# Performance work log

Hardware: AMD Instinct MI355X
Metric: run time of the kernel (lower is better)

## Reference

```python
import jax, jax.numpy as jnp
import numpy as np
import math

B, S, HID = 2, 2048, 2048
H, HK, D = 16, 4, 128          # query heads, kv heads, head_dim
R = 64                         # rope_dim = head_dim * partial_rotary_factor
EPS = 1e-6
THETA = 10000.0


def _rope_tables():
    inv_freq = 1.0 / (THETA ** (np.arange(0, R, 2, dtype=np.float32) / R))
    t = np.arange(S, dtype=np.float32)
    freqs = np.outer(t, inv_freq)                      # [S, R/2]
    emb = np.concatenate([freqs, freqs], axis=-1)      # [S, R]
    cos = np.broadcast_to(np.cos(emb)[None], (B, S, R)).copy()
    sin = np.broadcast_to(np.sin(emb)[None], (B, S, R)).copy()
    return jnp.asarray(cos), jnp.asarray(sin)


def setup_inputs() -> dict:
    key = jax.random.key(0)
    ks = jax.random.split(key, 3)
    cos, sin = _rope_tables()
    return {
        "hidden_states": jax.random.normal(ks[0], (B, S, HID), dtype=jnp.float32),
        "cos": cos,
        "sin": sin,
        "w_qkv": jax.random.normal(ks[1], ((H + 2 * HK) * D, HID), dtype=jnp.float32) * (HID ** -0.5),
        "q_ln_w": jnp.ones((D,), dtype=jnp.float32),
        "k_ln_w": jnp.ones((D,), dtype=jnp.float32),
        "w_dense": jax.random.normal(ks[2], (HID, H * D), dtype=jnp.float32) * ((H * D) ** -0.5),
    }


def _rms_norm(x, w):
    xf = x.astype(jnp.float32)
    var = jnp.mean(xf * xf, axis=-1, keepdims=True)
    return w * (xf * jax.lax.rsqrt(var + EPS)).astype(x.dtype)


def _rotate_half(x):
    x1, x2 = x[..., : x.shape[-1] // 2], x[..., x.shape[-1] // 2 :]
    return jnp.concatenate([-x2, x1], axis=-1)


def _apply_rope(q, k, cos, sin):
    # cos/sin: [B, S, R] -> [B, 1, S, R]; partial rotary on first R dims
    cos = cos[:, None, :, :]
    sin = sin[:, None, :, :]
    q_rot, q_pass = q[..., :R], q[..., R:]
    k_rot, k_pass = k[..., :R], k[..., R:]
    q_emb = q_rot * cos + _rotate_half(q_rot) * sin
    k_emb = k_rot * cos + _rotate_half(k_rot) * sin
    return (jnp.concatenate([q_emb, q_pass], axis=-1),
            jnp.concatenate([k_emb, k_pass], axis=-1))


def reference(hidden_states, cos, sin, w_qkv, q_ln_w, k_ln_w, w_dense):
    bsz, q_len, _ = hidden_states.shape
    qkv = jnp.einsum('bsh,oh->bso', hidden_states, w_qkv)            # [B,S,(H+2HK)*D]
    qkv = qkv.reshape(bsz, q_len, H + 2 * HK, D)
    q, k, v = jnp.split(qkv, [H, H + HK], axis=2)
    q = jnp.transpose(q, (0, 2, 1, 3))                               # [B,H,S,D]
    k = jnp.transpose(k, (0, 2, 1, 3))                               # [B,HK,S,D]
    v = jnp.transpose(v, (0, 2, 1, 3))

    q = _rms_norm(q, q_ln_w)
    k = _rms_norm(k, k_ln_w)
    q, k = _apply_rope(q, k, cos, sin)

    n_rep = H // HK
    k = jnp.repeat(k, n_rep, axis=1)                                 # [B,H,S,D]
    v = jnp.repeat(v, n_rep, axis=1)

    scores = jnp.einsum('bhqd,bhkd->bhqk', q, k) / math.sqrt(D)
    probs = jax.nn.softmax(scores.astype(jnp.float32), axis=-1).astype(q.dtype)
    attn = jnp.einsum('bhqk,bhkd->bhqd', probs, v)                   # [B,H,S,D]
    attn = jnp.transpose(attn, (0, 2, 1, 3)).reshape(bsz, q_len, H * D)
    return jnp.einsum('bsd,od->bso', attn, w_dense)                  # [B,S,HID]
```

## Files before the change

kernel.cpp:

```cpp
#include <hip/hip_runtime.h>
#include <hip/hip_bf16.h>
#include <math.h>

#define B_   2
#define S_   2048
#define HID_ 2048
#define H_   16
#define HK_  4
#define D_   128
#define NH_  24
#define QKVN 3072
#define R_   64

typedef __attribute__((ext_vector_type(8))) _Float16 h8;
typedef __attribute__((ext_vector_type(4))) _Float16 h4;
typedef __attribute__((ext_vector_type(2))) _Float16 h2;
typedef __attribute__((ext_vector_type(4))) float f4;

#define GLOAD16(gp, lp) __builtin_amdgcn_global_load_lds(                      \
    (const __attribute__((address_space(1))) void*)(gp),                       \
    (__attribute__((address_space(3))) void*)(lp), 16, 0, 0)

__global__ __launch_bounds__(256) void cvt3(
    const float* __restrict__ s0, _Float16* __restrict__ d0, int n0,
    const float* __restrict__ s1, _Float16* __restrict__ d1, int n1,
    const float* __restrict__ s2, _Float16* __restrict__ d2, int n2)
{
    int j = blockIdx.x * 256 + threadIdx.x;
    const float* s; _Float16* d;
    if (j < n0) { s = s0; d = d0; }
    else {
        j -= n0;
        if (j < n1) { s = s1; d = d1; }
        else { j -= n1; if (j >= n2) return; s = s2; d = d2; }
    }
    float4 a = ((const float4*)s)[j * 2];
    float4 b = ((const float4*)s)[j * 2 + 1];
    h8 h;
    h[0] = (_Float16)a.x; h[1] = (_Float16)a.y;
    h[2] = (_Float16)a.z; h[3] = (_Float16)a.w;
    h[4] = (_Float16)b.x; h[5] = (_Float16)b.y;
    h[6] = (_Float16)b.z; h[7] = (_Float16)b.w;
    ((h8*)d)[j] = h;
}

template<bool F16OUT>
__global__ __launch_bounds__(256) void gemm_f16(
    const _Float16* __restrict__ A, const _Float16* __restrict__ Bm,
    void* __restrict__ Cv, int M, int N, int K)
{
    __shared__ _Float16 Ast[128][64];
    __shared__ _Float16 Bst[128][64];

    const int tid = threadIdx.x;
    const int wave = tid >> 6, lane = tid & 63;
    const int l15 = lane & 15, l4 = lane >> 4;
    const int m0 = blockIdx.y * 128, n0 = blockIdx.x * 128;
    const int wm = (wave >> 1) * 64, wn = (wave & 1) * 64;

    f4 acc[16];
#pragma unroll
    for (int t = 0; t < 16; ++t) acc[t] = (f4){0.f, 0.f, 0.f, 0.f};

    const int srow = lane >> 3;
    const int scol = ((lane & 7) ^ srow) * 8;
    const int sw   = l15 & 7;

    for (int k0 = 0; k0 < K; k0 += 64) {
        __syncthreads();
#pragma unroll
        for (int t = 0; t < 4; ++t) {
            const int chunk = wave * 4 + t;
            const int grow  = chunk * 8 + srow;
            GLOAD16(A  + (size_t)(m0 + grow) * K + k0 + scol, &Ast[chunk * 8][0]);
            GLOAD16(Bm + (size_t)(n0 + grow) * K + k0 + scol, &Bst[chunk * 8][0]);
        }
        __syncthreads();

#pragma unroll
        for (int j = 0; j < 2; ++j) {
            h8 ahf[4], bhf[4];
#pragma unroll
            for (int i = 0; i < 4; ++i) {
                ahf[i] = *(const h8*)&Ast[wm + i * 16 + l15][((j * 4 + l4) ^ sw) * 8];
                bhf[i] = *(const h8*)&Bst[wn + i * 16 + l15][((j * 4 + l4) ^ sw) * 8];
            }
#pragma unroll
            for (int i = 0; i < 4; ++i)
#pragma unroll
                for (int jj = 0; jj < 4; ++jj)
                    acc[i * 4 + jj] = __builtin_amdgcn_mfma_f32_16x16x32_f16(
                        ahf[i], bhf[jj], acc[i * 4 + jj], 0, 0, 0);
        }
    }

#pragma unroll
    for (int i = 0; i < 4; ++i)
#pragma unroll
        for (int jj = 0; jj < 4; ++jj)
#pragma unroll
            for (int r = 0; r < 4; ++r) {
                int row = m0 + wm + i * 16 + l4 * 4 + r;
                int col = n0 + wn + jj * 16 + l15;
                if (F16OUT)
                    ((_Float16*)Cv)[(size_t)row * N + col] = (_Float16)acc[i * 4 + jj][r];
                else
                    ((float*)Cv)[(size_t)row * N + col] = acc[i * 4 + jj][r];
            }
}

__global__ __launch_bounds__(256) void norm_rope(
    const _Float16* __restrict__ qkv,
    const float* __restrict__ cosT, const float* __restrict__ sinT,
    const float* __restrict__ qw, const float* __restrict__ kw,
    _Float16* __restrict__ Qh_g, _Float16* __restrict__ Kh_g)
{
    const int tid = threadIdx.x;
    const int wave = tid >> 6, lane = tid & 63;
    const int h = blockIdx.x * 4 + wave;
    const int s = blockIdx.y, b = blockIdx.z;
    const size_t tok = (size_t)b * S_ + s;

    h2 xv = *(const h2*)(qkv + (tok * NH_ + h) * D_ + 2 * lane);
    float x0 = (float)xv[0], x1 = (float)xv[1];
    float ss = x0 * x0 + x1 * x1;
    ss += __shfl_xor(ss, 1);  ss += __shfl_xor(ss, 2);  ss += __shfl_xor(ss, 4);
    ss += __shfl_xor(ss, 8);  ss += __shfl_xor(ss, 16); ss += __shfl_xor(ss, 32);
    float scale = rsqrtf(ss * (1.f / 128.f) + 1e-6f);

    const float* wp = (h < 16) ? qw : kw;
    float2 wv = ((const float2*)wp)[lane];
    float y0 = x0 * scale * wv.x;
    float y1 = x1 * scale * wv.y;

    float p0 = __shfl_xor(y0, 16), p1 = __shfl_xor(y1, 16);
    if (lane < 32) {
        float2 cv = ((const float2*)(cosT + tok * R_))[lane];
        float2 sv = ((const float2*)(sinT + tok * R_))[lane];
        float sgn = (lane < 16) ? -1.f : 1.f;
        y0 = y0 * cv.x + sgn * p0 * sv.x;
        y1 = y1 * cv.y + sgn * p1 * sv.y;
    }

    if (h < 16) {
        const float QS = 0.08838834764831845f * 1.4426950408889634f;
        h2 o; o[0] = (_Float16)(y0 * QS); o[1] = (_Float16)(y1 * QS);
        *(h2*)(Qh_g + (((size_t)b * H_ + h) * S_ + s) * D_ + 2 * lane) = o;
    } else {
        h2 o; o[0] = (_Float16)y0; o[1] = (_Float16)y1;
        *(h2*)(Kh_g + (((size_t)b * HK_ + (h - 16)) * S_ + s) * D_ + 2 * lane) = o;
    }
}

__global__ __launch_bounds__(256) void vtrans(
    const _Float16* __restrict__ qkv, _Float16* __restrict__ Vt_g)
{
    __shared__ float Ts[64][132];
    const int tid = threadIdx.x;
    const int sb = blockIdx.x;
    const int bh = blockIdx.y;
    const int b = bh >> 2, kh = bh & 3;

#pragma unroll
    for (int t = 0; t < 4; ++t) {
        int e = (tid + 256 * t) * 8;
        int s = e >> 7, d = e & 127;
        const _Float16* p = qkv + (((size_t)(b * S_ + sb * 64 + s)) * NH_ + 20 + kh) * D_ + d;
        h8 v = *(const h8*)p;
#pragma unroll
        for (int u = 0; u < 8; ++u) Ts[s][d + u] = (float)v[u];
    }
    __syncthreads();

#pragma unroll
    for (int tt = 0; tt < 2; ++tt) {
        int dr = (tid >> 2) + 64 * tt;
        int sc = (tid & 3) * 16;
        _Float16 tmp[16];
#pragma unroll
        for (int i = 0; i < 16; ++i) tmp[i] = (_Float16)Ts[sc + i][dr];
        _Float16* outp = Vt_g + ((size_t)bh * D_ + dr) * S_ + sb * 64 + sc;
        *(h8*)outp       = *(h8*)&tmp[0];
        *(h8*)(outp + 8) = *(h8*)&tmp[8];
    }
}

__global__ __launch_bounds__(256, 2) void flash_mfma(
    const _Float16* __restrict__ Qh_g, const _Float16* __restrict__ Kh_g,
    const _Float16* __restrict__ Vt_g, _Float16* __restrict__ Ao)
{
    __shared__ _Float16 Ksh[2][64][128];
    __shared__ _Float16 Vsh[2][128][64];
    __shared__ _Float16 Ps [128][64];

    const int tid = threadIdx.x;
    const int wave = tid >> 6, lane = tid & 63;
    const int l15 = lane & 15, l4 = lane >> 4;
    const int qb = blockIdx.x, h = blockIdx.y, b = blockIdx.z;
    const int kh = h >> 2;
    const int key = l15 & 7;

    h8 qf[2][4];
#pragma unroll
    for (int i = 0; i < 2; ++i) {
        const _Float16* qrow = Qh_g +
            (((size_t)b * H_ + h) * S_ + qb * 128 + wave * 32 + i * 16 + l15) * D_;
#pragma unroll
        for (int j = 0; j < 4; ++j)
            qf[i][j] = *(const h8*)(qrow + j * 32 + l4 * 8);
    }

    f4 o[2][8];
#pragma unroll
    for (int i = 0; i < 2; ++i)
#pragma unroll
        for (int t = 0; t < 8; ++t) o[i][t] = (f4){0.f, 0.f, 0.f, 0.f};
    float l_part[2] = {0.f, 0.f};

    const size_t kvoff = ((size_t)b * HK_ + kh) * S_ * D_;
    const _Float16* kg = Kh_g + kvoff;
    const _Float16* vg = Vt_g + kvoff;

    int krow[4], ksrc[4], vrow[4], vsrc[4];
#pragma unroll
    for (int t = 0; t < 4; ++t) {
        krow[t] = wave * 16 + t * 4 + (lane >> 4);
        ksrc[t] = ((lane & 15) ^ (krow[t] & 7)) * 8;
        vrow[t] = wave * 32 + t * 8 + (lane >> 3);
        vsrc[t] = ((lane & 7) ^ (vrow[t] & 7)) * 8;
    }

    auto STAGE = [&](int bf, int kb) {
#pragma unroll
        for (int t = 0; t < 4; ++t)
            GLOAD16(kg + (size_t)(kb * 64 + krow[t]) * D_ + ksrc[t],
                    &Ksh[bf][wave * 16 + t * 4][0]);
#pragma unroll
        for (int t = 0; t < 4; ++t)
            GLOAD16(vg + (size_t)vrow[t] * S_ + kb * 64 + vsrc[t],
                    &Vsh[bf][wave * 32 + t * 8][0]);
    };

    STAGE(0, 0);
    int cur = 0;

    for (int kb = 0; kb < S_ / 64; ++kb) {
        __syncthreads();
        if (kb + 1 < S_ / 64) STAGE(cur ^ 1, kb + 1);

        f4 acc[4][2];
#pragma unroll
        for (int c = 0; c < 4; ++c)
#pragma unroll
            for (int i = 0; i < 2; ++i)
                acc[c][i] = (f4){-8.f, -8.f, -8.f, -8.f};
#pragma unroll
        for (int j = 0; j < 4; ++j) {
#pragma unroll
            for (int c = 0; c < 4; ++c) {
                h8 kf = *(const h8*)&Ksh[cur][c * 16 + l15][((j * 4 + l4) ^ key) * 8];
#pragma unroll
                for (int i = 0; i < 2; ++i)
                    acc[c][i] = __builtin_amdgcn_mfma_f32_16x16x32_f16(
                        kf, qf[i][j], acc[c][i], 0, 0, 0);
            }
        }

#pragma unroll
        for (int c = 0; c < 4; ++c) {
#pragma unroll
            for (int i = 0; i < 2; ++i) {
                h4 pk;
#pragma unroll
                for (int r = 0; r < 4; ++r) {
                    float e_ = exp2f(acc[c][i][r]);
                    l_part[i] += e_;
                    pk[r] = (_Float16)e_;
                }
                int g = 2 * c + (l4 >> 1);
                *(h4*)&Ps[wave * 32 + i * 16 + l15][(g ^ key) * 8 + (l4 & 1) * 4] = pk;
            }
        }

#pragma unroll
        for (int s2 = 0; s2 < 2; ++s2) {
            int gc = ((s2 * 4 + l4) ^ key) * 8;
            h8 pf0 = *(const h8*)&Ps[wave * 32 + l15][gc];
            h8 pf1 = *(const h8*)&Ps[wave * 32 + 16 + l15][gc];
#pragma unroll
            for (int t = 0; t < 8; ++t) {
                h8 vf = *(const h8*)&Vsh[cur][t * 16 + l15][gc];
                o[0][t] = __builtin_amdgcn_mfma_f32_16x16x32_f16(pf0, vf, o[0][t], 0, 0, 0);
                o[1][t] = __builtin_amdgcn_mfma_f32_16x16x32_f16(pf1, vf, o[1][t], 0, 0, 0);
            }
        }
        cur ^= 1;
    }

    float Linv[2];
#pragma unroll
    for (int i = 0; i < 2; ++i) {
        float l = l_part[i];
        l += __shfl_xor(l, 16);
        l += __shfl_xor(l, 32);
        Linv[i] = 1.f / l;
    }
#pragma unroll
    for (int i = 0; i < 2; ++i) {
        float inv[4];
#pragma unroll
        for (int r = 0; r < 4; ++r) inv[r] = __shfl(Linv[i], l4 * 4 + r);
#pragma unroll
        for (int t = 0; t < 8; ++t) {
#pragma unroll
            for (int r = 0; r < 4; ++r) {
                int row = qb * 128 + wave * 32 + i * 16 + l4 * 4 + r;
                Ao[((size_t)b * S_ + row) * (H_ * D_) + h * D_ + t * 16 + l15] =
                    (_Float16)(o[i][t][r] * inv[r]);
            }
        }
    }
}

extern "C" void kernel_launch(void* const* d_in, const int* in_sizes, int n_in,
                              void* d_out, int out_size, void* d_ws, size_t ws_size,
                              hipStream_t stream)
{
    const float* hidden  = (const float*)d_in[0];
    const float* cosT    = (const float*)d_in[1];
    const float* sinT    = (const float*)d_in[2];
    const float* w_qkv   = (const float*)d_in[3];
    const float* q_ln    = (const float*)d_in[4];
    const float* k_ln    = (const float*)d_in[5];
    const float* w_dense = (const float*)d_in[6];
    float* out = (float*)d_out;

    char* w = (char*)d_ws;
    _Float16* qkv16 = (_Float16*)w;
    _Float16* Qh    = (_Float16*)(w + 25165824);
    _Float16* Kh    = (_Float16*)(w + 41943040);
    _Float16* Vt    = (_Float16*)(w + 46137344);
    _Float16* wdense16 = (_Float16*)(w + 54525952);
    _Float16* hidden16 = Qh;
    _Float16* wqkv16   = Kh;
    _Float16* attn16   = qkv16;

    cvt3<<<9216, 256, 0, stream>>>(hidden,  hidden16, 1048576,
                                   w_qkv,   wqkv16,   786432,
                                   w_dense, wdense16, 524288);

    gemm_f16<true><<<dim3(QKVN / 128, (B_ * S_) / 128), 256, 0, stream>>>(
        hidden16, wqkv16, qkv16, B_ * S_, QKVN, HID_);

    norm_rope<<<dim3(5, S_, B_), 256, 0, stream>>>(
        qkv16, cosT, sinT, q_ln, k_ln, Qh, Kh);

    vtrans<<<dim3(S_ / 64, B_ * HK_), 256, 0, stream>>>(qkv16, Vt);

    flash_mfma<<<dim3(S_ / 128, H_, B_), 256, 0, stream>>>(Qh, Kh, Vt, attn16);

    gemm_f16<false><<<dim3(HID_ / 128, (B_ * S_) / 128), 256, 0, stream>>>(
        attn16, wdense16, out, B_ * S_, HID_, H_ * D_);
}
```

Measured before the change: 354.5 us.

## Split flash attention waves across query and key halves with LDS reduction

The flash kernel now splits its four waves as 2 query groups x 2 key groups. Each wave covers 64 query rows and 32 of the 64 keys per block, so each Q fragment is reused against more K/V loads, and the two key-half partial outputs and row sums are combined through shared memory at the end. The GEMM inner loop also raises wave priority around the MFMA burst. The trade-off is more live accumulator registers per wave (o grows from 16 to 32 f4), which may lower occupancy or cause spills, plus an extra LDS reduction and barrier in the epilogue.

After: 375.0 us. 1.06x slower.

```diff
diff --git a/kernel.cpp b/kernel.cpp
--- a/kernel.cpp
+++ b/kernel.cpp
@@ -85,12 +85,14 @@
                 ahf[i] = *(const h8*)&Ast[wm + i * 16 + l15][((j * 4 + l4) ^ sw) * 8];
                 bhf[i] = *(const h8*)&Bst[wn + i * 16 + l15][((j * 4 + l4) ^ sw) * 8];
             }
+            __builtin_amdgcn_s_setprio(1);
 #pragma unroll
             for (int i = 0; i < 4; ++i)
 #pragma unroll
                 for (int jj = 0; jj < 4; ++jj)
                     acc[i * 4 + jj] = __builtin_amdgcn_mfma_f32_16x16x32_f16(
                         ahf[i], bhf[jj], acc[i * 4 + jj], 0, 0, 0);
+            __builtin_amdgcn_s_setprio(0);
         }
     }
 
@@ -189,33 +191,35 @@
     const _Float16* __restrict__ Qh_g, const _Float16* __restrict__ Kh_g,
     const _Float16* __restrict__ Vt_g, _Float16* __restrict__ Ao)
 {
-    __shared__ _Float16 Ksh[2][64][128];
-    __shared__ _Float16 Vsh[2][128][64];
-    __shared__ _Float16 Ps [128][64];
+    __shared__ char smem[81920];
+    auto Ksh = (_Float16 (*)[64][128])smem;
+    auto Vsh = (_Float16 (*)[128][64])(smem + 32768);
+    auto Ps  = (_Float16 (*)[64])(smem + 65536);
 
     const int tid = threadIdx.x;
     const int wave = tid >> 6, lane = tid & 63;
     const int l15 = lane & 15, l4 = lane >> 4;
+    const int wq = wave >> 1, wk = wave & 1;
     const int qb = blockIdx.x, h = blockIdx.y, b = blockIdx.z;
     const int kh = h >> 2;
     const int key = l15 & 7;
 
-    h8 qf[2][4];
-#pragma unroll
-    for (int i = 0; i < 2; ++i) {
+    h8 qf[4][4];
+#pragma unroll
+    for (int i = 0; i < 4; ++i) {
         const _Float16* qrow = Qh_g +
-            (((size_t)b * H_ + h) * S_ + qb * 128 + wave * 32 + i * 16 + l15) * D_;
+            (((size_t)b * H_ + h) * S_ + qb * 128 + wq * 64 + i * 16 + l15) * D_;
 #pragma unroll
         for (int j = 0; j < 4; ++j)
             qf[i][j] = *(const h8*)(qrow + j * 32 + l4 * 8);
     }
 
-    f4 o[2][8];
-#pragma unroll
-    for (int i = 0; i < 2; ++i)
+    f4 o[4][8];
+#pragma unroll
+    for (int i = 0; i < 4; ++i)
 #pragma unroll
         for (int t = 0; t < 8; ++t) o[i][t] = (f4){0.f, 0.f, 0.f, 0.f};
-    float l_part[2] = {0.f, 0.f};
+    float l_part[4] = {0.f, 0.f, 0.f, 0.f};
 
     const size_t kvoff = ((size_t)b * HK_ + kh) * S_ * D_;
     const _Float16* kg = Kh_g + kvoff;
@@ -248,28 +252,29 @@
         __syncthreads();
         if (kb + 1 < S_ / 64) STAGE(cur ^ 1, kb + 1);
 
-        f4 acc[4][2];
-#pragma unroll
-        for (int c = 0; c < 4; ++c)
-#pragma unroll
-            for (int i = 0; i < 2; ++i)
+        f4 acc[2][4];
+#pragma unroll
+        for (int c = 0; c < 2; ++c)
+#pragma unroll
+            for (int i = 0; i < 4; ++i)
                 acc[c][i] = (f4){-8.f, -8.f, -8.f, -8.f};
 #pragma unroll
         for (int j = 0; j < 4; ++j) {
 #pragma unroll
-            for (int c = 0; c < 4; ++c) {
-                h8 kf = *(const h8*)&Ksh[cur][c * 16 + l15][((j * 4 + l4) ^ key) * 8];
-#pragma unroll
-                for (int i = 0; i < 2; ++i)
+            for (int c = 0; c < 2; ++c) {
+                h8 kf = *(const h8*)&Ksh[cur][wk * 32 + c * 16 + l15]
+                                          [((j * 4 + l4) ^ key) * 8];
+#pragma unroll
+                for (int i = 0; i < 4; ++i)
                     acc[c][i] = __builtin_amdgcn_mfma_f32_16x16x32_f16(
                         kf, qf[i][j], acc[c][i], 0, 0, 0);
             }
         }
 
 #pragma unroll
-        for (int c = 0; c < 4; ++c) {
-#pragma unroll
-            for (int i = 0; i < 2; ++i) {
+        for (int c = 0; c < 2; ++c) {
+#pragma unroll
+            for (int i = 0; i < 4; ++i) {
                 h4 pk;
 #pragma unroll
                 for (int r = 0; r < 4; ++r) {
@@ -277,47 +282,71 @@
                     l_part[i] += e_;
                     pk[r] = (_Float16)e_;
                 }
-                int g = 2 * c + (l4 >> 1);
-                *(h4*)&Ps[wave * 32 + i * 16 + l15][(g ^ key) * 8 + (l4 & 1) * 4] = pk;
-            }
-        }
-
-#pragma unroll
-        for (int s2 = 0; s2 < 2; ++s2) {
-            int gc = ((s2 * 4 + l4) ^ key) * 8;
-            h8 pf0 = *(const h8*)&Ps[wave * 32 + l15][gc];
-            h8 pf1 = *(const h8*)&Ps[wave * 32 + 16 + l15][gc];
+                int g = wk * 4 + c * 2 + (l4 >> 1);
+                *(h4*)&Ps[wq * 64 + i * 16 + l15][(g ^ key) * 8 + (l4 & 1) * 4] = pk;
+            }
+        }
+
+        {
+            const int gc = ((wk * 4 + l4) ^ key) * 8;
+            h8 pf[4];
+#pragma unroll
+            for (int i = 0; i < 4; ++i)
+                pf[i] = *(const h8*)&Ps[wq * 64 + i * 16 + l15][gc];
 #pragma unroll
             for (int t = 0; t < 8; ++t) {
                 h8 vf = *(const h8*)&Vsh[cur][t * 16 + l15][gc];
-                o[0][t] = __builtin_amdgcn_mfma_f32_16x16x32_f16(pf0, vf, o[0][t], 0, 0, 0);
-                o[1][t] = __builtin_amdgcn_mfma_f32_16x16x32_f16(pf1, vf, o[1][t], 0, 0, 0);
+#pragma unroll
+                for (int i = 0; i < 4; ++i)
+                    o[i][t] = __builtin_amdgcn_mfma_f32_16x16x32_f16(
+                        pf[i], vf, o[i][t], 0, 0, 0);
             }
         }
         cur ^= 1;
     }
 
-    float Linv[2];
-#pragma unroll
-    for (int i = 0; i < 2; ++i) {
+    float lp[4];
+#pragma unroll
+    for (int i = 0; i < 4; ++i) {
         float l = l_part[i];
         l += __shfl_xor(l, 16);
         l += __shfl_xor(l, 32);
-        Linv[i] = 1.f / l;
-    }
-#pragma unroll
-    for (int i = 0; i < 2; ++i) {
-        float inv[4];
-#pragma unroll
-        for (int r = 0; r < 4; ++r) inv[r] = __shfl(Linv[i], l4 * 4 + r);
-#pragma unroll
-        for (int t = 0; t < 8; ++t) {
-#pragma unroll
-            for (int r = 0; r < 4; ++r) {
-                int row = qb * 128 + wave * 32 + i * 16 + l4 * 4 + r;
-                Ao[((size_t)b * S_ + row) * (H_ * D_) + h * D_ + t * 16 + l15] =
-                    (_Float16)(o[i][t][r] * inv[r]);
-            }
+        lp[i] = l;
+    }
+
+    __syncthreads();
+    float (*ex)[128] = (float (*)[128])smem;
+    float* Ls = (float*)(smem + 65536);
+
+    if (wk == 1) {
+#pragma unroll
+        for (int i = 0; i < 4; ++i) {
+#pragma unroll
+            for (int t = 0; t < 8; ++t)
+#pragma unroll
+                for (int r = 0; r < 4; ++r)
+                    ex[wq * 64 + i * 16 + l4 * 4 + r][t * 16 + l15] = o[i][t][r];
+            if (l4 == 0) Ls[wq * 64 + i * 16 + l15] = lp[i];
+        }
+    }
+    __syncthreads();
+    if (wk == 0) {
+#pragma unroll
+        for (int i = 0; i < 4; ++i) {
+            float Linv = 1.f / (lp[i] + Ls[wq * 64 + i * 16 + l15]);
+            float inv[4];
+#pragma unroll
+            for (int r = 0; r < 4; ++r) inv[r] = __shfl(Linv, l4 * 4 + r);
+#pragma unroll
+            for (int t = 0; t < 8; ++t)
+#pragma unroll
+                for (int r = 0; r < 4; ++r) {
+                    int qrow = wq * 64 + i * 16 + l4 * 4 + r;
+                    int row = qb * 128 + qrow;
+                    float v = o[i][t][r] + ex[qrow][t * 16 + l15];
+                    Ao[((size_t)b * S_ + row) * (H_ * D_) + h * D_ + t * 16 + l15] =
+                        (_Float16)(v * inv[r]);
+                }
         }
     }
 }
```

## Fuse RMSNorm, RoPE and V transpose into QKV GEMM epilogue

Applied to the files above, without the earlier changes.

The QKV projection GEMM now normalizes each head tile in its epilogue. It reduces the squared sums across the two N-half waves through shared memory, then applies RoPE and the query scale before writing Q/K in head-major layout. It also writes V directly transposed. This drops the separate norm_rope and vtrans kernels and the fp16 qkv intermediate round-trip. The change also adds s_setprio around the MFMA blocks in both GEMMs, and the epilogue writes Q/K with scattered 2-byte stores, which may be less coalesced than before.

New measurement: 335.7 us. -5.3%, faster.

```diff
diff --git a/kernel.cpp b/kernel.cpp
--- a/kernel.cpp
+++ b/kernel.cpp
@@ -44,10 +44,166 @@
     ((h8*)d)[j] = h;
 }
 
-template<bool F16OUT>
-__global__ __launch_bounds__(256) void gemm_f16(
+__global__ __launch_bounds__(256) void gemm_qkv(
     const _Float16* __restrict__ A, const _Float16* __restrict__ Bm,
-    void* __restrict__ Cv, int M, int N, int K)
+    const float* __restrict__ cosT, const float* __restrict__ sinT,
+    const float* __restrict__ qw, const float* __restrict__ kw,
+    _Float16* __restrict__ Qh_g, _Float16* __restrict__ Kh_g,
+    _Float16* __restrict__ Vt_g)
+{
+    __shared__ _Float16 Ast[128][64];
+    __shared__ _Float16 Bst[128][64];
+    __shared__ float exch[2][128];
+
+    const int tid = threadIdx.x;
+    const int wave = tid >> 6, lane = tid & 63;
+    const int l15 = lane & 15, l4 = lane >> 4;
+    const int h  = blockIdx.x;
+    const int m0 = blockIdx.y * 128;
+    const int n0 = h * 128;
+    const int wm = (wave >> 1) * 64, wn = (wave & 1) * 64;
+    const int K = HID_;
+
+    f4 acc[16];
+#pragma unroll
+    for (int t = 0; t < 16; ++t) acc[t] = (f4){0.f, 0.f, 0.f, 0.f};
+
+    const int srow = lane >> 3;
+    const int scol = ((lane & 7) ^ srow) * 8;
+    const int sw   = l15 & 7;
+
+    for (int k0 = 0; k0 < K; k0 += 64) {
+        __syncthreads();
+#pragma unroll
+        for (int t = 0; t < 4; ++t) {
+            const int chunk = wave * 4 + t;
+            const int grow  = chunk * 8 + srow;
+            GLOAD16(A  + (size_t)(m0 + grow) * K + k0 + scol, &Ast[chunk * 8][0]);
+            GLOAD16(Bm + (size_t)(n0 + grow) * K + k0 + scol, &Bst[chunk * 8][0]);
+        }
+        __syncthreads();
+
+#pragma unroll
+        for (int j = 0; j < 2; ++j) {
+            h8 ahf[4], bhf[4];
+#pragma unroll
+            for (int i = 0; i < 4; ++i) {
+                ahf[i] = *(const h8*)&Ast[wm + i * 16 + l15][((j * 4 + l4) ^ sw) * 8];
+                bhf[i] = *(const h8*)&Bst[wn + i * 16 + l15][((j * 4 + l4) ^ sw) * 8];
+            }
+            __builtin_amdgcn_s_setprio(1);
+#pragma unroll
+            for (int i = 0; i < 4; ++i)
+#pragma unroll
+                for (int jj = 0; jj < 4; ++jj)
+                    acc[i * 4 + jj] = __builtin_amdgcn_mfma_f32_16x16x32_f16(
+                        ahf[i], bhf[jj], acc[i * 4 + jj], 0, 0, 0);
+            __builtin_amdgcn_s_setprio(0);
+        }
+    }
+
+    const int bb = m0 >> 11;
+    const int s0 = m0 & 2047;
+
+    if (h < 20) {
+        float sq[4][4];
+#pragma unroll
+        for (int i = 0; i < 4; ++i)
+#pragma unroll
+            for (int r = 0; r < 4; ++r) {
+                float s = 0.f;
+#pragma unroll
+                for (int jj = 0; jj < 4; ++jj) {
+                    float v = acc[i * 4 + jj][r];
+                    s += v * v;
+                }
+                s += __shfl_xor(s, 1);
+                s += __shfl_xor(s, 2);
+                s += __shfl_xor(s, 4);
+                s += __shfl_xor(s, 8);
+                sq[i][r] = s;
+            }
+        const int half = wn >> 6;
+        if (l15 == 0) {
+#pragma unroll
+            for (int i = 0; i < 4; ++i)
+#pragma unroll
+                for (int r = 0; r < 4; ++r)
+                    exch[half][wm + i * 16 + l4 * 4 + r] = sq[i][r];
+        }
+        __syncthreads();
+
+        const float* wln = (h < 16) ? qw : kw;
+        float wv[4];
+#pragma unroll
+        for (int jj = 0; jj < 4; ++jj) wv[jj] = wln[wn + jj * 16 + l15];
+
+        const float QS = 0.08838834764831845f * 1.4426950408889634f;
+
+#pragma unroll
+        for (int i = 0; i < 4; ++i) {
+#pragma unroll
+            for (int r = 0; r < 4; ++r) {
+                const int row = wm + i * 16 + l4 * 4 + r;
+                const int s  = s0 + row;
+                float tot = sq[i][r] + exch[half ^ 1][row];
+                float scale = rsqrtf(tot * (1.f / 128.f) + 1e-6f);
+                float y[4];
+#pragma unroll
+                for (int jj = 0; jj < 4; ++jj)
+                    y[jj] = acc[i * 4 + jj][r] * scale * wv[jj];
+
+                float yr[4];
+                if (wn == 0) {
+                    const float* cp = cosT + ((size_t)bb * S_ + s) * R_;
+                    const float* sp = sinT + ((size_t)bb * S_ + s) * R_;
+                    float cs[4], sn[4];
+#pragma unroll
+                    for (int jj = 0; jj < 4; ++jj) {
+                        cs[jj] = cp[jj * 16 + l15];
+                        sn[jj] = sp[jj * 16 + l15];
+                    }
+                    yr[0] = y[0] * cs[0] - y[2] * sn[0];
+                    yr[1] = y[1] * cs[1] - y[3] * sn[1];
+                    yr[2] = y[2] * cs[2] + y[0] * sn[2];
+                    yr[3] = y[3] * cs[3] + y[1] * sn[3];
+                } else {
+#pragma unroll
+                    for (int jj = 0; jj < 4; ++jj) yr[jj] = y[jj];
+                }
+
+                if (h < 16) {
+                    _Float16* qp = Qh_g + (((size_t)bb * H_ + h) * S_ + s) * D_;
+#pragma unroll
+                    for (int jj = 0; jj < 4; ++jj)
+                        qp[wn + jj * 16 + l15] = (_Float16)(yr[jj] * QS);
+                } else {
+                    _Float16* kp = Kh_g + (((size_t)bb * HK_ + (h - 16)) * S_ + s) * D_;
+#pragma unroll
+                    for (int jj = 0; jj < 4; ++jj)
+                        kp[wn + jj * 16 + l15] = (_Float16)yr[jj];
+                }
+            }
+        }
+    } else {
+        const size_t vbase = ((size_t)bb * HK_ + (h - 20)) * D_ * S_;
+#pragma unroll
+        for (int i = 0; i < 4; ++i)
+#pragma unroll
+            for (int jj = 0; jj < 4; ++jj) {
+                h4 pk;
+#pragma unroll
+                for (int r = 0; r < 4; ++r) pk[r] = (_Float16)acc[i * 4 + jj][r];
+                const int d = wn + jj * 16 + l15;
+                const int s = s0 + wm + i * 16 + l4 * 4;
+                *(h4*)(Vt_g + vbase + (size_t)d * S_ + s) = pk;
+            }
+    }
+}
+
+__global__ __launch_bounds__(256) void gemm_dense(
+    const _Float16* __restrict__ A, const _Float16* __restrict__ Bm,
+    float* __restrict__ Cv, int M, int N, int K)
 {
     __shared__ _Float16 Ast[128][64];
     __shared__ _Float16 Bst[128][64];
@@ -85,12 +241,14 @@
                 ahf[i] = *(const h8*)&Ast[wm + i * 16 + l15][((j * 4 + l4) ^ sw) * 8];
                 bhf[i] = *(const h8*)&Bst[wn + i * 16 + l15][((j * 4 + l4) ^ sw) * 8];
             }
+            __builtin_amdgcn_s_setprio(1);
 #pragma unroll
             for (int i = 0; i < 4; ++i)
 #pragma unroll
                 for (int jj = 0; jj < 4; ++jj)
                     acc[i * 4 + jj] = __builtin_amdgcn_mfma_f32_16x16x32_f16(
                         ahf[i], bhf[jj], acc[i * 4 + jj], 0, 0, 0);
+            __builtin_amdgcn_s_setprio(0);
         }
     }
 
@@ -102,87 +260,8 @@
             for (int r = 0; r < 4; ++r) {
                 int row = m0 + wm + i * 16 + l4 * 4 + r;
                 int col = n0 + wn + jj * 16 + l15;
-                if (F16OUT)
-                    ((_Float16*)Cv)[(size_t)row * N + col] = (_Float16)acc[i * 4 + jj][r];
-                else
-                    ((float*)Cv)[(size_t)row * N + col] = acc[i * 4 + jj][r];
-            }
-}
-
-__global__ __launch_bounds__(256) void norm_rope(
-    const _Float16* __restrict__ qkv,
-    const float* __restrict__ cosT, const float* __restrict__ sinT,
-    const float* __restrict__ qw, const float* __restrict__ kw,
-    _Float16* __restrict__ Qh_g, _Float16* __restrict__ Kh_g)
-{
-    const int tid = threadIdx.x;
-    const int wave = tid >> 6, lane = tid & 63;
-    const int h = blockIdx.x * 4 + wave;
-    const int s = blockIdx.y, b = blockIdx.z;
-    const size_t tok = (size_t)b * S_ + s;
-
-    h2 xv = *(const h2*)(qkv + (tok * NH_ + h) * D_ + 2 * lane);
-    float x0 = (float)xv[0], x1 = (float)xv[1];
-    float ss = x0 * x0 + x1 * x1;
-    ss += __shfl_xor(ss, 1);  ss += __shfl_xor(ss, 2);  ss += __shfl_xor(ss, 4);
-    ss += __shfl_xor(ss, 8);  ss += __shfl_xor(ss, 16); ss += __shfl_xor(ss, 32);
-    float scale = rsqrtf(ss * (1.f / 128.f) + 1e-6f);
-
-    const float* wp = (h < 16) ? qw : kw;
-    float2 wv = ((const float2*)wp)[lane];
-    float y0 = x0 * scale * wv.x;
-    float y1 = x1 * scale * wv.y;
-
-    float p0 = __shfl_xor(y0, 16), p1 = __shfl_xor(y1, 16);
-    if (lane < 32) {
-        float2 cv = ((const float2*)(cosT + tok * R_))[lane];
-        float2 sv = ((const float2*)(sinT + tok * R_))[lane];
-        float sgn = (lane < 16) ? -1.f : 1.f;
-        y0 = y0 * cv.x + sgn * p0 * sv.x;
-        y1 = y1 * cv.y + sgn * p1 * sv.y;
-    }
-
-    if (h < 16) {
-        const float QS = 0.08838834764831845f * 1.4426950408889634f;
-        h2 o; o[0] = (_Float16)(y0 * QS); o[1] = (_Float16)(y1 * QS);
-        *(h2*)(Qh_g + (((size_t)b * H_ + h) * S_ + s) * D_ + 2 * lane) = o;
-    } else {
-        h2 o; o[0] = (_Float16)y0; o[1] = (_Float16)y1;
-        *(h2*)(Kh_g + (((size_t)b * HK_ + (h - 16)) * S_ + s) * D_ + 2 * lane) = o;
-    }
-}
-
-__global__ __launch_bounds__(256) void vtrans(
-    const _Float16* __restrict__ qkv, _Float16* __restrict__ Vt_g)
-{
-    __shared__ float Ts[64][132];
-    const int tid = threadIdx.x;
-    const int sb = blockIdx.x;
-    const int bh = blockIdx.y;
-    const int b = bh >> 2, kh = bh & 3;
-
-#pragma unroll
-    for (int t = 0; t < 4; ++t) {
-        int e = (tid + 256 * t) * 8;
-        int s = e >> 7, d = e & 127;
-        const _Float16* p = qkv + (((size_t)(b * S_ + sb * 64 + s)) * NH_ + 20 + kh) * D_ + d;
-        h8 v = *(const h8*)p;
-#pragma unroll
-        for (int u = 0; u < 8; ++u) Ts[s][d + u] = (float)v[u];
-    }
-    __syncthreads();
-
-#pragma unroll
-    for (int tt = 0; tt < 2; ++tt) {
-        int dr = (tid >> 2) + 64 * tt;
-        int sc = (tid & 3) * 16;
-        _Float16 tmp[16];
-#pragma unroll
-        for (int i = 0; i < 16; ++i) tmp[i] = (_Float16)Ts[sc + i][dr];
-        _Float16* outp = Vt_g + ((size_t)bh * D_ + dr) * S_ + sb * 64 + sc;
-        *(h8*)outp       = *(h8*)&tmp[0];
-        *(h8*)(outp + 8) = *(h8*)&tmp[8];
-    }
+                Cv[(size_t)row * N + col] = acc[i * 4 + jj][r];
+            }
 }
 
 __global__ __launch_bounds__(256, 2) void flash_mfma(
@@ -336,29 +415,23 @@
     float* out = (float*)d_out;
 
     char* w = (char*)d_ws;
-    _Float16* qkv16 = (_Float16*)w;
-    _Float16* Qh    = (_Float16*)(w + 25165824);
-    _Float16* Kh    = (_Float16*)(w + 41943040);
-    _Float16* Vt    = (_Float16*)(w + 46137344);
-    _Float16* wdense16 = (_Float16*)(w + 54525952);
-    _Float16* hidden16 = Qh;
-    _Float16* wqkv16   = Kh;
-    _Float16* attn16   = qkv16;
+    _Float16* attn16   = (_Float16*)w;
+    _Float16* hidden16 = (_Float16*)(w + 16777216);
+    _Float16* wqkv16   = (_Float16*)(w + 33554432);
+    _Float16* Qh       = (_Float16*)(w + 46137344);
+    _Float16* Kh       = (_Float16*)(w + 62914560);
+    _Float16* Vt       = (_Float16*)(w + 67108864);
+    _Float16* wdense16 = (_Float16*)(w + 71303168);
 
     cvt3<<<9216, 256, 0, stream>>>(hidden,  hidden16, 1048576,
                                    w_qkv,   wqkv16,   786432,
                                    w_dense, wdense16, 524288);
 
-    gemm_f16<true><<<dim3(QKVN / 128, (B_ * S_) / 128), 256, 0, stream>>>(
-        hidden16, wqkv16, qkv16, B_ * S_, QKVN, HID_);
-
-    norm_rope<<<dim3(5, S_, B_), 256, 0, stream>>>(
-        qkv16, cosT, sinT, q_ln, k_ln, Qh, Kh);
-
-    vtrans<<<dim3(S_ / 64, B_ * HK_), 256, 0, stream>>>(qkv16, Vt);
+    gemm_qkv<<<dim3(NH_, (B_ * S_) / 128), 256, 0, stream>>>(
+        hidden16, wqkv16, cosT, sinT, q_ln, k_ln, Qh, Kh, Vt);
 
     flash_mfma<<<dim3(S_ / 128, H_, B_), 256, 0, stream>>>(Qh, Kh, Vt, attn16);
 
-    gemm_f16<false><<<dim3(HID_ / 128, (B_ * S_) / 128), 256, 0, stream>>>(
+    gemm_dense<<<dim3(HID_ / 128, (B_ * S_) / 128), 256, 0, stream>>>(
         attn16, wdense16, out, B_ * S_, HID_, H_ * D_);
 }
```
